# Kernel optimization log

Measured on AMD Instinct MI355X. Metric: run time of the kernel, lower is better.

Reference implementation:

```python
import jax, jax.numpy as jnp
import numpy as np

N = 50000
E = 800000
D = 128


def setup_inputs() -> dict:
    key = jax.random.key(0)
    ks = jax.random.split(key, 6)
    x = jax.random.normal(ks[0], (N, D), dtype=jnp.float32)
    W_self = jax.random.normal(ks[1], (D, D), dtype=jnp.float32) * (1.0 / np.sqrt(D))
    b_self = jax.random.normal(ks[2], (D,), dtype=jnp.float32) * 0.01
    W_neigh = jax.random.normal(ks[3], (D, D), dtype=jnp.float32) * (1.0 / np.sqrt(D))
    src = jax.random.randint(ks[4], (E,), 0, N, dtype=jnp.int32)
    dst = jax.random.randint(ks[5], (E,), 0, N, dtype=jnp.int32)
    # Row-normalized adjacency: weight of edge (src -> dst) is 1/deg(dst)
    deg = jax.ops.segment_sum(jnp.ones((E,), jnp.float32), dst, num_segments=N)
    edge_w = 1.0 / jnp.maximum(deg, 1.0)[dst]
    return {"x": x, "W_self": W_self, "b_self": b_self, "W_neigh": W_neigh,
            "edge_w": edge_w, "src": src, "dst": dst}


def reference(x, W_self, b_self, W_neigh, edge_w, src, dst):
    n = x.shape[0]
    # neigh = A @ x  (row-normalized sparse adjacency as weighted edge list)
    msgs = x[src] * edge_w[:, None]               # (E, D) gather + scale
    neigh = jax.ops.segment_sum(msgs, dst, num_segments=n)  # (N, D) scatter-add
    # lin_self(x) + lin_neigh(neigh)  (torch Linear: y = x @ W.T + b)
    return x @ W_self.T + b_self + neigh @ W_neigh.T
```

## Files before the change

### kernel.cpp

```cpp
#include <hip/hip_runtime.h>
#include <hip/hip_bf16.h>

#define N_NODES 50000
#define N_EDGES 800000
#define DIM 128

#define RSH 6
#define RNODES 64
#define NRANGE 782
#define CH 4096
#define NB 196
#define NTOT (NRANGE * NB)
#define NSCANB ((NTOT + 1023) / 1024)
#define BCAP 64
#define MM_BLOCKS ((N_NODES + 127) / 128)

typedef __attribute__((ext_vector_type(8))) short bf16x8;
typedef __attribute__((ext_vector_type(4))) float f32x4;

union BU8 { uint4 u; bf16x8 b; };

static __device__ __forceinline__ ushort f2bf(float f) {
    __hip_bfloat16 h = __float2bfloat16(f);
    return *reinterpret_cast<ushort*>(&h);
}
static __device__ __forceinline__ uint pack2(float a, float b) {
    return (uint)f2bf(a) | ((uint)f2bf(b) << 16);
}
static __device__ __forceinline__ float bflo(uint u) { return __uint_as_float(u << 16); }
static __device__ __forceinline__ float bfhi(uint u) { return __uint_as_float(u & 0xffff0000u); }

__global__ __launch_bounds__(256, 2) void mmhist_k(const float* __restrict__ x,
                                                   const float* __restrict__ Ws,
                                                   const float* __restrict__ Wn,
                                                   const float* __restrict__ bias,
                                                   const int* __restrict__ dst,
                                                   float* __restrict__ out,
                                                   ushort* __restrict__ Yn,
                                                   int* __restrict__ histg,
                                                   int* __restrict__ ovfcnt) {
    __shared__ ushort wlds[32768];
    int tid = threadIdx.x;

    if (blockIdx.x >= MM_BLOCKS) {
        int b = blockIdx.x - MM_BLOCKS;
        if (b == 0 && tid == 0) *ovfcnt = 0;
        int* h = (int*)wlds;
        for (int i = tid; i < NRANGE; i += 256) h[i] = 0;
        __syncthreads();
        int e0 = b * CH;
        int n = N_EDGES - e0; if (n > CH) n = CH;
        for (int i = tid; i < n; i += 256) atomicAdd(&h[dst[e0 + i] >> RSH], 1);
        __syncthreads();
        for (int i = tid; i < NRANGE; i += 256) histg[b * NRANGE + i] = h[i];
        return;
    }

    int lane = tid & 63;
    int w    = tid >> 6;
    int lr   = lane & 15;
    int g    = lane >> 4;
    int myrow0 = blockIdx.x * 128 + w * 32;

    bf16x8 a[2][4];
#pragma unroll
    for (int rt = 0; rt < 2; ++rt) {
        int row = myrow0 + rt * 16 + lr;
        bool ok = row < N_NODES;
        const float* ap = x + (size_t)row * 128;
#pragma unroll
        for (int kf = 0; kf < 4; ++kf) {
            float4 f0 = make_float4(0.f, 0.f, 0.f, 0.f), f1 = f0;
            if (ok) {
                f0 = *(const float4*)(ap + kf * 32 + g * 8);
                f1 = *(const float4*)(ap + kf * 32 + g * 8 + 4);
            }
            BU8 u;
            u.u.x = pack2(f0.x, f0.y); u.u.y = pack2(f0.z, f0.w);
            u.u.z = pack2(f1.x, f1.y); u.u.w = pack2(f1.z, f1.w);
            a[rt][kf] = u.b;
        }
    }

#pragma unroll
    for (int i = 0; i < 16; ++i) {
        int f = i * 256 + tid;
        int r = f >> 4, c = f & 15;
        const float* wsrc = ((r < 128) ? (Ws + (size_t)r * 128)
                                       : (Wn + (size_t)(r - 128) * 128)) + c * 8;
        float4 f0 = *(const float4*)(wsrc);
        float4 f1 = *(const float4*)(wsrc + 4);
        uint4 u;
        u.x = pack2(f0.x, f0.y); u.y = pack2(f0.z, f0.w);
        u.z = pack2(f1.x, f1.y); u.w = pack2(f1.z, f1.w);
        *(uint4*)(&wlds[r * 128 + ((c ^ (r & 7)) * 8)]) = u;
    }
    __syncthreads();

    f32x4 acc[2][16];
#pragma unroll
    for (int rt = 0; rt < 2; ++rt)
#pragma unroll
        for (int nt = 0; nt < 16; ++nt) acc[rt][nt] = (f32x4){0.f, 0.f, 0.f, 0.f};

#pragma unroll
    for (int nt = 0; nt < 16; ++nt) {
        int row = nt * 16 + lr;
#pragma unroll
        for (int kf = 0; kf < 4; ++kf) {
            int chunk = kf * 4 + g;
            bf16x8 b = *(const bf16x8*)(&wlds[row * 128 + ((chunk ^ (lr & 7)) * 8)]);
            acc[0][nt] = __builtin_amdgcn_mfma_f32_16x16x32_bf16(a[0][kf], b, acc[0][nt], 0, 0, 0);
            acc[1][nt] = __builtin_amdgcn_mfma_f32_16x16x32_bf16(a[1][kf], b, acc[1][nt], 0, 0, 0);
        }
    }

#pragma unroll
    for (int nt = 0; nt < 16; ++nt) {
        int col = nt * 16 + lr;
        float bv = (col < 128) ? bias[col] : 0.f;
#pragma unroll
        for (int rt = 0; rt < 2; ++rt) {
            int rowb = myrow0 + rt * 16 + g * 4;
#pragma unroll
            for (int j = 0; j < 4; ++j) {
                int row = rowb + j;
                if (row < N_NODES) {
                    if (col < 128)
                        out[(size_t)row * 128 + col] = acc[rt][nt][j] + bv;
                    else
                        Yn[(size_t)row * 128 + (col - 128)] = f2bf(acc[rt][nt][j]);
                }
            }
        }
    }
}

__global__ __launch_bounds__(1024) void scanA_k(const int* __restrict__ histg,
                                                int* __restrict__ off,
                                                int* __restrict__ bsum) {
    __shared__ int lds[1024];
    int t = threadIdx.x;
    int c = blockIdx.x * 1024 + t;
    int v = 0;
    if (c < NTOT) {
        int r = c / NB, b = c - r * NB;
        v = histg[b * NRANGE + r];
    }
    lds[t] = v;
    __syncthreads();
    for (int s = 1; s < 1024; s <<= 1) {
        int add = (t >= s) ? lds[t - s] : 0;
        __syncthreads();
        lds[t] += add;
        __syncthreads();
    }
    if (c < NTOT) off[c] = lds[t] - v;
    if (t == 1023) bsum[blockIdx.x] = lds[1023];
}

__global__ __launch_bounds__(256) void scatter_k(const int* __restrict__ src,
                                                 const int* __restrict__ dst,
                                                 const int* __restrict__ off,
                                                 const int* __restrict__ bsum,
                                                 uint* __restrict__ buf) {
    __shared__ int cur[NRANGE];
    __shared__ int sb[256];
    int t = threadIdx.x, b = blockIdx.x;

    int v = (t < NSCANB) ? bsum[t] : 0;
    sb[t] = v;
    __syncthreads();
    for (int s = 1; s < 256; s <<= 1) {
        int add = (t >= s) ? sb[t - s] : 0;
        __syncthreads();
        sb[t] += add;
        __syncthreads();
    }
    sb[t] -= v;
    __syncthreads();

    for (int i = t; i < NRANGE; i += 256) {
        int c = i * NB + b;
        cur[i] = off[c] + sb[c >> 10];
    }
    __syncthreads();

    int e0 = b * CH;
    int n = N_EDGES - e0; if (n > CH) n = CH;
    for (int i = t; i < n; i += 256) {
        int e = e0 + i;
        int d = dst[e];
        int r = d >> RSH;
        int pos = atomicAdd(&cur[r], 1);
        buf[pos] = ((uint)src[e] << RSH) | (uint)(d & (RNODES - 1));
    }
}

__global__ __launch_bounds__(512) void agg4_k(const ushort* __restrict__ Yn,
                                              const uint* __restrict__ buf,
                                              const int* __restrict__ off,
                                              const int* __restrict__ bsum,
                                              float* __restrict__ out,
                                              int* __restrict__ count,
                                              int* __restrict__ ovfcnt,
                                              int2* __restrict__ ovf) {
    __shared__ ushort bkt[RNODES][BCAP];
    __shared__ int cnt[RNODES];
    __shared__ int sb[256];
    int r = blockIdx.x;
    int t = threadIdx.x;
    if (t < RNODES) cnt[t] = 0;

    int v = 0;
    if (t < 256) {
        v = (t < NSCANB) ? bsum[t] : 0;
        sb[t] = v;
    }
    __syncthreads();
    for (int s = 1; s < 256; s <<= 1) {
        int add = 0;
        if (t < 256 && t >= s) add = sb[t - s];
        __syncthreads();
        if (t < 256) sb[t] += add;
        __syncthreads();
    }
    if (t < 256) sb[t] -= v;
    __syncthreads();

    int c0 = r * NB;
    int start = off[c0] + sb[c0 >> 10];
    int end;
    if (r == NRANGE - 1) end = N_EDGES;
    else { int c1 = (r + 1) * NB; end = off[c1] + sb[c1 >> 10]; }

    for (int i = start + t; i < end; i += 512) {
        uint p = buf[i];
        int local = (int)(p & (RNODES - 1));
        int s = (int)(p >> RSH);
        int pos = atomicAdd(&cnt[local], 1);
        if (pos < BCAP) {
            bkt[local][pos] = (ushort)s;
        } else {
            int o = atomicAdd(ovfcnt, 1);
            ovf[o] = make_int2(s, r * RNODES + local);
        }
    }
    __syncthreads();

    int lane = t & 63;
    int wv = t >> 6;
    int g = lane >> 4;
    int c8 = (lane & 15) * 8;

#pragma unroll 1
    for (int q = 0; q < 8; ++q) {
        int n = wv * 8 + q;
        int gnode = r * RNODES + n;
        if (gnode >= N_NODES) continue;
        int deg = cnt[n];
        if (lane == 0) count[gnode] = deg;
        int m = (deg < BCAP) ? deg : BCAP;
        int sreg = (lane < m) ? (int)bkt[n][lane] : 0;

        float acc0 = 0.f, acc1 = 0.f, acc2 = 0.f, acc3 = 0.f;
        float acc4 = 0.f, acc5 = 0.f, acc6 = 0.f, acc7 = 0.f;

#define ACC8(v)                                        \
    do {                                               \
        acc0 += bflo(v.x); acc1 += bfhi(v.x);          \
        acc2 += bflo(v.y); acc3 += bfhi(v.y);          \
        acc4 += bflo(v.z); acc5 += bfhi(v.z);          \
        acc6 += bflo(v.w); acc7 += bfhi(v.w);          \
    } while (0)

        int j = 0;
        for (; j + 4 <= m; j += 4) {
            int s = __shfl(sreg, j + g);
            uint4 vv = *(const uint4*)(Yn + (size_t)s * 128 + c8);
            ACC8(vv);
        }
        if (j < m) {
            int jj = j + g;
            bool valid = jj < m;
            int s = __shfl(sreg, valid ? jj : j);
            uint4 vv = *(const uint4*)(Yn + (size_t)s * 128 + c8);
            if (valid) ACC8(vv);
        }
#undef ACC8

#define RED(a) do { a += __shfl_xor(a, 16); a += __shfl_xor(a, 32); } while (0)
        RED(acc0); RED(acc1); RED(acc2); RED(acc3);
        RED(acc4); RED(acc5); RED(acc6); RED(acc7);
#undef RED

        if (lane < 16) {
            float scale = 1.0f / (float)(deg > 0 ? deg : 1);
            float* orow = out + (size_t)gnode * 128 + c8;
            float4 o0 = *(const float4*)(orow);
            float4 o1 = *(const float4*)(orow + 4);
            o0.x += scale * acc0; o0.y += scale * acc1;
            o0.z += scale * acc2; o0.w += scale * acc3;
            o1.x += scale * acc4; o1.y += scale * acc5;
            o1.z += scale * acc6; o1.w += scale * acc7;
            *(float4*)(orow) = o0;
            *(float4*)(orow + 4) = o1;
        }
    }
}

__global__ void ovf_k(const ushort* __restrict__ Yn, const int* __restrict__ count,
                      const int* __restrict__ ovfcnt, const int2* __restrict__ ovf,
                      float* __restrict__ out) {
    int n = *ovfcnt;
    for (int i = blockIdx.x; i < n; i += gridDim.x) {
        int2 e = ovf[i];
        int s = e.x, d = e.y;
        float scale = 1.0f / (float)max(count[d], 1);
        int c = threadIdx.x;
        float v = __uint_as_float(((uint)Yn[(size_t)s * 128 + c]) << 16);
        atomicAdd(&out[(size_t)d * 128 + c], scale * v);
    }
}

extern "C" void kernel_launch(void* const* d_in, const int* in_sizes, int n_in,
                              void* d_out, int out_size, void* d_ws, size_t ws_size,
                              hipStream_t stream) {
    const float* x       = (const float*)d_in[0];
    const float* W_self  = (const float*)d_in[1];
    const float* b_self  = (const float*)d_in[2];
    const float* W_neigh = (const float*)d_in[3];
    const int* src = (const int*)d_in[5];
    const int* dst = (const int*)d_in[6];
    float* out = (float*)d_out;

    char* ws = (char*)d_ws;
    ushort* Yn     = (ushort*)(ws);
    int*    histg  = (int*)(ws + 12800000);
    int*    off    = (int*)(ws + 13413088);
    uint*   buf    = (uint*)(ws + 14026176);
    int*    count  = (int*)(ws + 17226176);
    int*    ovfcnt = (int*)(ws + 17426176);
    int*    bsum   = (int*)(ws + 17426192);
    int2*   ovf    = (int2*)(ws + 17427216);

    mmhist_k<<<MM_BLOCKS + NB, 256, 0, stream>>>(x, W_self, W_neigh, b_self, dst,
                                                 out, Yn, histg, ovfcnt);

    scanA_k<<<NSCANB, 1024, 0, stream>>>(histg, off, bsum);
    scatter_k<<<NB, 256, 0, stream>>>(src, dst, off, bsum, buf);

    agg4_k<<<NRANGE, 512, 0, stream>>>(Yn, buf, off, bsum, out, count, ovfcnt, ovf);

    ovf_k<<<64, 128, 0, stream>>>(Yn, count, ovfcnt, ovf, out);
}
```

Before: 84.80 us.

## Overlap edge scatter with matmul instead of histogram; unroll gather by two

The histogram moves into its own small kernel and the scan runs right after it. The heavier scatter pass then shares a launch with the dense matmul blocks, so the bucketing work overlaps the GEMM instead of running as a separate serialized kernel. The aggregation loop also issues two row gathers per iteration to raise memory-level parallelism. The trade-off is that the histogram now runs alone before the matmul, and the scatter blocks compete with the GEMM blocks for CUs.

After: 81.99 us. -3.3%, faster.

```diff
diff --git a/kernel.cpp b/kernel.cpp
--- a/kernel.cpp
+++ b/kernel.cpp
@@ -30,29 +30,90 @@
 static __device__ __forceinline__ float bflo(uint u) { return __uint_as_float(u << 16); }
 static __device__ __forceinline__ float bfhi(uint u) { return __uint_as_float(u & 0xffff0000u); }
 
-__global__ __launch_bounds__(256, 2) void mmhist_k(const float* __restrict__ x,
+__global__ __launch_bounds__(256) void hist_k(const int* __restrict__ dst,
+                                              int* __restrict__ histg,
+                                              int* __restrict__ ovfcnt) {
+    __shared__ int h[NRANGE];
+    int t = threadIdx.x, b = blockIdx.x;
+    if (b == 0 && t == 0) *ovfcnt = 0;
+    for (int i = t; i < NRANGE; i += 256) h[i] = 0;
+    __syncthreads();
+    int e0 = b * CH;
+    int n = N_EDGES - e0; if (n > CH) n = CH;
+    for (int i = t; i < n; i += 256) atomicAdd(&h[dst[e0 + i] >> RSH], 1);
+    __syncthreads();
+    for (int i = t; i < NRANGE; i += 256) histg[b * NRANGE + i] = h[i];
+}
+
+__global__ __launch_bounds__(1024) void scanA_k(const int* __restrict__ histg,
+                                                int* __restrict__ off,
+                                                int* __restrict__ bsum) {
+    __shared__ int lds[1024];
+    int t = threadIdx.x;
+    int c = blockIdx.x * 1024 + t;
+    int v = 0;
+    if (c < NTOT) {
+        int r = c / NB, b = c - r * NB;
+        v = histg[b * NRANGE + r];
+    }
+    lds[t] = v;
+    __syncthreads();
+    for (int s = 1; s < 1024; s <<= 1) {
+        int add = (t >= s) ? lds[t - s] : 0;
+        __syncthreads();
+        lds[t] += add;
+        __syncthreads();
+    }
+    if (c < NTOT) off[c] = lds[t] - v;
+    if (t == 1023) bsum[blockIdx.x] = lds[1023];
+}
+
+__global__ __launch_bounds__(256, 2) void mmscat_k(const float* __restrict__ x,
                                                    const float* __restrict__ Ws,
                                                    const float* __restrict__ Wn,
                                                    const float* __restrict__ bias,
+                                                   const int* __restrict__ src,
                                                    const int* __restrict__ dst,
+                                                   const int* __restrict__ off,
+                                                   const int* __restrict__ bsum,
                                                    float* __restrict__ out,
                                                    ushort* __restrict__ Yn,
-                                                   int* __restrict__ histg,
-                                                   int* __restrict__ ovfcnt) {
+                                                   uint* __restrict__ buf) {
     __shared__ ushort wlds[32768];
     int tid = threadIdx.x;
 
     if (blockIdx.x >= MM_BLOCKS) {
         int b = blockIdx.x - MM_BLOCKS;
-        if (b == 0 && tid == 0) *ovfcnt = 0;
-        int* h = (int*)wlds;
-        for (int i = tid; i < NRANGE; i += 256) h[i] = 0;
-        __syncthreads();
+        int* cur = (int*)wlds;
+        int* sb  = (int*)wlds + NRANGE;
+
+        int v = (tid < NSCANB) ? bsum[tid] : 0;
+        sb[tid] = v;
+        __syncthreads();
+        for (int s = 1; s < 256; s <<= 1) {
+            int add = (tid >= s) ? sb[tid - s] : 0;
+            __syncthreads();
+            sb[tid] += add;
+            __syncthreads();
+        }
+        sb[tid] -= v;
+        __syncthreads();
+
+        for (int i = tid; i < NRANGE; i += 256) {
+            int c = i * NB + b;
+            cur[i] = off[c] + sb[c >> 10];
+        }
+        __syncthreads();
+
         int e0 = b * CH;
         int n = N_EDGES - e0; if (n > CH) n = CH;
-        for (int i = tid; i < n; i += 256) atomicAdd(&h[dst[e0 + i] >> RSH], 1);
-        __syncthreads();
-        for (int i = tid; i < NRANGE; i += 256) histg[b * NRANGE + i] = h[i];
+        for (int i = tid; i < n; i += 256) {
+            int e = e0 + i;
+            int d = dst[e];
+            int r = d >> RSH;
+            int pos = atomicAdd(&cur[r], 1);
+            buf[pos] = ((uint)src[e] << RSH) | (uint)(d & (RNODES - 1));
+        }
         return;
     }
 
@@ -133,67 +194,6 @@
                 }
             }
         }
-    }
-}
-
-__global__ __launch_bounds__(1024) void scanA_k(const int* __restrict__ histg,
-                                                int* __restrict__ off,
-                                                int* __restrict__ bsum) {
-    __shared__ int lds[1024];
-    int t = threadIdx.x;
-    int c = blockIdx.x * 1024 + t;
-    int v = 0;
-    if (c < NTOT) {
-        int r = c / NB, b = c - r * NB;
-        v = histg[b * NRANGE + r];
-    }
-    lds[t] = v;
-    __syncthreads();
-    for (int s = 1; s < 1024; s <<= 1) {
-        int add = (t >= s) ? lds[t - s] : 0;
-        __syncthreads();
-        lds[t] += add;
-        __syncthreads();
-    }
-    if (c < NTOT) off[c] = lds[t] - v;
-    if (t == 1023) bsum[blockIdx.x] = lds[1023];
-}
-
-__global__ __launch_bounds__(256) void scatter_k(const int* __restrict__ src,
-                                                 const int* __restrict__ dst,
-                                                 const int* __restrict__ off,
-                                                 const int* __restrict__ bsum,
-                                                 uint* __restrict__ buf) {
-    __shared__ int cur[NRANGE];
-    __shared__ int sb[256];
-    int t = threadIdx.x, b = blockIdx.x;
-
-    int v = (t < NSCANB) ? bsum[t] : 0;
-    sb[t] = v;
-    __syncthreads();
-    for (int s = 1; s < 256; s <<= 1) {
-        int add = (t >= s) ? sb[t - s] : 0;
-        __syncthreads();
-        sb[t] += add;
-        __syncthreads();
-    }
-    sb[t] -= v;
-    __syncthreads();
-
-    for (int i = t; i < NRANGE; i += 256) {
-        int c = i * NB + b;
-        cur[i] = off[c] + sb[c >> 10];
-    }
-    __syncthreads();
-
-    int e0 = b * CH;
-    int n = N_EDGES - e0; if (n > CH) n = CH;
-    for (int i = t; i < n; i += 256) {
-        int e = e0 + i;
-        int d = dst[e];
-        int r = d >> RSH;
-        int pos = atomicAdd(&cur[r], 1);
-        buf[pos] = ((uint)src[e] << RSH) | (uint)(d & (RNODES - 1));
     }
 }
 
@@ -275,6 +275,14 @@
     } while (0)
 
         int j = 0;
+        for (; j + 8 <= m; j += 8) {
+            int s0 = __shfl(sreg, j + g);
+            int s1 = __shfl(sreg, j + 4 + g);
+            uint4 v0 = *(const uint4*)(Yn + (size_t)s0 * 128 + c8);
+            uint4 v1 = *(const uint4*)(Yn + (size_t)s1 * 128 + c8);
+            ACC8(v0);
+            ACC8(v1);
+        }
         for (; j + 4 <= m; j += 4) {
             int s = __shfl(sreg, j + g);
             uint4 vv = *(const uint4*)(Yn + (size_t)s * 128 + c8);
@@ -344,11 +352,12 @@
     int*    bsum   = (int*)(ws + 17426192);
     int2*   ovf    = (int2*)(ws + 17427216);
 
-    mmhist_k<<<MM_BLOCKS + NB, 256, 0, stream>>>(x, W_self, W_neigh, b_self, dst,
-                                                 out, Yn, histg, ovfcnt);
-
+    hist_k<<<NB, 256, 0, stream>>>(dst, histg, ovfcnt);
     scanA_k<<<NSCANB, 1024, 0, stream>>>(histg, off, bsum);
-    scatter_k<<<NB, 256, 0, stream>>>(src, dst, off, bsum, buf);
+
+    mmscat_k<<<MM_BLOCKS + NB, 256, 0, stream>>>(x, W_self, W_neigh, b_self,
+                                                 src, dst, off, bsum,
+                                                 out, Yn, buf);
 
     agg4_k<<<NRANGE, 512, 0, stream>>>(Yn, buf, off, bsum, out, count, ovfcnt, ovf);
 
```
